# Kernel optimization log

Hardware: AMD Instinct MI355X
Metric: run time of the kernel (lower is better)

## Reference

```python
import jax, jax.numpy as jnp
import numpy as np

B, S, E, D, DE = 8, 128, 50, 300, 50  # batch, seq, edge_dim, gcn_dim, dep_embed_dim
EPS = 1e-6


def setup_inputs() -> dict:
    key = jax.random.key(0)
    ks = jax.random.split(key, 9)
    weight_prob_softmax = jax.nn.softmax(jax.random.normal(ks[0], (B, S, S, E)), axis=2)
    weight_adj = jax.random.normal(ks[1], (B, S, S, E))
    gcn_inputs = jax.random.normal(ks[2], (B, S, D))
    # self-loop added to adjacency after permute -> [B, E, S, S]; identity loops
    self_loop = jnp.broadcast_to(jnp.eye(S, dtype=jnp.float32), (B, E, S, S))
    W_w = jax.random.normal(ks[3], (D, D)) * 0.05          # gcn linear (in, out)
    W_b = jnp.zeros((D,))
    ln_a = jnp.ones((D,))
    ln_b = jnp.zeros((D,))
    refine_W = jax.random.normal(ks[4], (2 * D + 3 * E, DE)) * 0.05  # (750, 50)
    refine_b = jnp.zeros((DE,))
    return {
        "weight_prob_softmax": weight_prob_softmax,
        "weight_adj": weight_adj,
        "gcn_inputs": gcn_inputs,
        "self_loop": self_loop,
        "W_w": W_w, "W_b": W_b,
        "ln_a": ln_a, "ln_b": ln_b,
        "refine_W": refine_W, "refine_b": refine_b,
    }


def reference(weight_prob_softmax, weight_adj, gcn_inputs, self_loop,
              W_w, W_b, ln_a, ln_b, refine_W, refine_b):
    b, s, d = gcn_inputs.shape
    e = weight_prob_softmax.shape[-1]
    # [B,S,S,E] -> [B,E,S,S], add self loops
    wps = jnp.transpose(weight_prob_softmax, (0, 3, 1, 2)) + self_loop
    # per-relation-channel message passing: Ax[b,e,i,:] = sum_j wps[b,e,i,j] * x[b,j,:]
    Ax = jnp.einsum('beij,bjd->beid', wps, gcn_inputs)
    Ax = Ax.mean(axis=1)  # avg pooling over edge channels -> [B,S,D]
    h = Ax @ W_w + W_b
    # LayerNorm with unbiased std (torch x.std default) and (std + eps)
    mean = h.mean(axis=-1, keepdims=True)
    var_unbiased = jnp.sum((h - mean) ** 2, axis=-1, keepdims=True) / (d - 1)
    std = jnp.sqrt(var_unbiased)
    h = ln_a * (h - mean) / (std + EPS) + ln_b
    node = jax.nn.relu(h)  # [B,S,D]
    # node1[b,i,j] = node[b,j]; node2[b,i,j] = node[b,i]
    node1 = jnp.broadcast_to(node[:, None, :, :], (b, s, s, d))
    node2 = jnp.broadcast_to(node[:, :, None, :], (b, s, s, d))
    # diagonal edge features: [B,E,S] -> [B,S,E]
    diag = jnp.transpose(jnp.diagonal(weight_adj, axis1=1, axis2=2), (0, 2, 1))
    edge_i = jnp.broadcast_to(diag[:, None, :, :], (b, s, s, e))  # edge_i[b,i,j]=diag[b,j]
    edge_j = jnp.broadcast_to(diag[:, :, None, :], (b, s, s, e))  # edge_j[b,i,j]=diag[b,i]
    feat = jnp.concatenate([weight_adj, edge_i, edge_j, node1, node2], axis=-1)
    edge_out = feat @ refine_W + refine_b  # [B,S,S,DE]
    return node, edge_out
```

## Files before the change

kernel.cpp:

```cpp
#include <hip/hip_runtime.h>
#include <hip/hip_bf16.h>


typedef __bf16 bf16x8 __attribute__((ext_vector_type(8)));
typedef float f32x4 __attribute__((ext_vector_type(4)));
typedef float f32x2 __attribute__((ext_vector_type(2)));

__device__ __forceinline__ unsigned short f2bf(float f) {
    __hip_bfloat16 h = __float2bfloat16(f);
    union { __hip_bfloat16 h; unsigned short u; } c; c.h = h; return c.u;
}

__global__ void __launch_bounds__(1024, 8) k_node(
    const float* __restrict__ wps,
    const float* __restrict__ wa,
    const float* __restrict__ x,
    const float* __restrict__ Ww,
    const float* __restrict__ Wb,
    const float* __restrict__ lna,
    const float* __restrict__ lnb,
    const float* __restrict__ Rw,
    const float* __restrict__ rb,
    float* __restrict__ node_out,
    float* __restrict__ R1, float* __restrict__ R2)
{
    __shared__ __align__(16) float axp[6400];
    __shared__ __align__(16) float axm2[608];
    __shared__ __align__(16) float Mlt[256];
    __shared__ __align__(16) float srcL[704];
    __shared__ float red1[10], red2[10], stats[4];

    int tid = threadIdx.x;
    int row0 = blockIdx.x * 2;
    int b = row0 >> 7, i0 = row0 & 127;

    {
        const float2* p2 = (const float2*)(wps + (size_t)row0 * 6400);
        for (int idx = tid; idx < 6400; idx += 1024) {
            float2 v = p2[idx];
            axp[idx] = v.x + v.y;
        }
    }
    if (tid < 100) {
        int r = tid / 50, e = tid % 50;
        srcL[e * 2 + r] = wa[((size_t)(row0 + r) * 128 + (i0 + r)) * 50 + e];
    }
    __syncthreads();
    if (tid < 256) {
        int r = tid >> 7, j = tid & 127;
        const float* pp = &axp[tid * 25];
        float s = 0.f;
#pragma unroll
        for (int n = 0; n < 25; ++n) s += pp[n];
        Mlt[j * 2 + r] = s * (1.0f / 50.0f) + (((i0 + r) == j) ? 1.0f : 0.0f);
    }
    __syncthreads();

    int t = tid & 255, g = tid >> 8;
    bool has2 = (t < 44);
    int d1 = has2 ? 256 + t : 299;

    {
        f32x2 a0 = {0.f, 0.f}, a1 = {0.f, 0.f};
        const float* xp = x + (size_t)b * 38400;
        int j0 = g * 32;
#pragma unroll 8
        for (int jj = 0; jj < 32; ++jj) {
            int j = j0 + jj;
            f32x2 m2 = *(const f32x2*)&Mlt[j * 2];
            a0 += m2 * xp[j * 300 + t];
            a1 += m2 * xp[j * 300 + d1];
        }
        *(f32x2*)&axp[g * 608 + t * 2] = a0;
        if (has2) *(f32x2*)&axp[g * 608 + d1 * 2] = a1;
    }
    __syncthreads();
    if (tid < 300) {
        f32x2 s = *(f32x2*)&axp[tid * 2]        + *(f32x2*)&axp[608 + tid * 2]
                + *(f32x2*)&axp[1216 + tid * 2] + *(f32x2*)&axp[1824 + tid * 2];
        *(f32x2*)&axm2[tid * 2] = s;
    }
    __syncthreads();

    {
        f32x2 h0 = {0.f, 0.f}, h1 = {0.f, 0.f};
        int kb = g * 75, ke = kb + 75;
#pragma unroll 5
        for (int k = kb; k < ke; ++k) {
            f32x2 m2 = *(const f32x2*)&axm2[k * 2];
            h0 += m2 * Ww[k * 300 + t];
            h1 += m2 * Ww[k * 300 + d1];
        }
        *(f32x2*)&axp[g * 608 + t * 2] = h0;
        if (has2) *(f32x2*)&axp[g * 608 + d1 * 2] = h1;
    }
    __syncthreads();

    f32x2 hv = {0.f, 0.f};
    int wvi = tid >> 6, lane = tid & 63;
    if (tid < 320) {
        if (tid < 300) {
            hv = *(f32x2*)&axp[tid * 2]        + *(f32x2*)&axp[608 + tid * 2]
               + *(f32x2*)&axp[1216 + tid * 2] + *(f32x2*)&axp[1824 + tid * 2];
            hv += Wb[tid];
        }
        float s1r[2], s2r[2];
#pragma unroll
        for (int r = 0; r < 2; ++r) { s1r[r] = hv[r]; s2r[r] = hv[r] * hv[r]; }
        for (int off = 32; off; off >>= 1) {
#pragma unroll
            for (int r = 0; r < 2; ++r) {
                s1r[r] += __shfl_down(s1r[r], off);
                s2r[r] += __shfl_down(s2r[r], off);
            }
        }
        if (lane == 0) {
#pragma unroll
            for (int r = 0; r < 2; ++r) { red1[wvi * 2 + r] = s1r[r]; red2[wvi * 2 + r] = s2r[r]; }
        }
    }
    __syncthreads();
    if (tid < 2) {
        float s1 = 0.f, s2 = 0.f;
#pragma unroll
        for (int w = 0; w < 5; ++w) { s1 += red1[w * 2 + tid]; s2 += red2[w * 2 + tid]; }
        float mean = s1 * (1.0f / 300.0f);
        float var = (s2 - 300.0f * mean * mean) * (1.0f / 299.0f);
        var = fmaxf(var, 0.0f);
        stats[tid * 2] = mean;
        stats[tid * 2 + 1] = 1.0f / (sqrtf(var) + 1e-6f);
    }
    __syncthreads();

    if (tid < 300) {
        float la = lna[tid], lb = lnb[tid];
        f32x2 nv;
#pragma unroll
        for (int r = 0; r < 2; ++r) {
            float v = la * (hv[r] - stats[r * 2]) * stats[r * 2 + 1] + lb;
            v = fmaxf(v, 0.f);
            nv[r] = v;
            node_out[(size_t)(row0 + r) * 300 + tid] = v;
        }
        *(f32x2*)&srcL[(50 + tid) * 2] = nv;
    }
    __syncthreads();

    if (tid < 700) {
        int p = tid / 50, k = tid % 50;
        f32x2 r1a = {0.f, 0.f}, r2a = {0.f, 0.f};
        int ib = p * 25;
#pragma unroll 5
        for (int idx = ib; idx < ib + 25; ++idx) {
            f32x2 sv = *(const f32x2*)&srcL[idx * 2];
            float w1, w2;
            if (idx < 50) { w1 = Rw[(50 + idx) * 50 + k]; w2 = Rw[(100 + idx) * 50 + k]; }
            else { int d = idx - 50; w1 = Rw[(150 + d) * 50 + k]; w2 = Rw[(450 + d) * 50 + k]; }
            r1a += sv * w1;
            r2a += sv * w2;
        }
        *(f32x2*)&axp[(p * 50 + k) * 2] = r1a;
        *(f32x2*)&axp[2800 + (p * 50 + k) * 2] = r2a;
    }
    __syncthreads();
    if (tid < 100) {
        int r = tid / 50, k = tid % 50;
        float s1 = 0.f, s2 = rb[k];
#pragma unroll
        for (int p = 0; p < 14; ++p) {
            s1 += axp[(p * 50 + k) * 2 + r];
            s2 += axp[2800 + (p * 50 + k) * 2 + r];
        }
        R1[(size_t)(row0 + r) * 50 + k] = s1;
        R2[(size_t)(row0 + r) * 50 + k] = s2;
    }
}

__global__ void __launch_bounds__(256) k_edge(
    const float* __restrict__ wa,
    const float* __restrict__ Rw,
    const float* __restrict__ R1, const float* __restrict__ R2,
    float* __restrict__ eout)
{
    __shared__ __align__(16) unsigned char smem[27648];
    unsigned short* waA  = (unsigned short*)smem;
    unsigned short* rwBT = (unsigned short*)(smem + 18432);
    float* outF = (float*)smem;
    int tid = threadIdx.x;
    int bi = blockIdx.x;
    int b = bi >> 7;

    for (int idx = tid; idx < 2304; idx += 256) ((unsigned int*)rwBT)[idx] = 0u;
    for (int idx = tid; idx < 1408; idx += 256) {
        int j = idx / 11, c = idx % 11;
        *((unsigned int*)(waA + j * 72 + 50) + c) = 0u;
    }
    __syncthreads();

    const float2* wap = (const float2*)(wa + (size_t)bi * 6400);
    for (int idx = tid; idx < 3200; idx += 256) {
        float2 v = wap[idx];
        int f = idx * 2;
        int j = f / 50, e = f % 50;
        unsigned int pack = (unsigned int)f2bf(v.x) | ((unsigned int)f2bf(v.y) << 16);
        *(unsigned int*)(waA + j * 72 + e) = pack;
    }
    for (int idx = tid; idx < 2500; idx += 256) {
        int e = idx / 50, kk = idx % 50;
        rwBT[kk * 72 + e] = f2bf(Rw[idx]);
    }
    __syncthreads();

    int lane = tid & 63, wv = tid >> 6;
    int q = lane >> 4, lr = lane & 15;
    f32x4 acc[2][4] = {};

#pragma unroll
    for (int ks = 0; ks < 2; ++ks) {
        int e0 = ks * 32 + q * 8;
        bf16x8 a0 = *(const bf16x8*)&waA[(wv * 32 + lr) * 72 + e0];
        bf16x8 a1 = *(const bf16x8*)&waA[(wv * 32 + 16 + lr) * 72 + e0];
#pragma unroll
        for (int nt = 0; nt < 4; ++nt) {
            bf16x8 bb = *(const bf16x8*)&rwBT[(nt * 16 + lr) * 72 + e0];
            acc[0][nt] = __builtin_amdgcn_mfma_f32_16x16x32_bf16(a0, bb, acc[0][nt], 0, 0, 0);
            acc[1][nt] = __builtin_amdgcn_mfma_f32_16x16x32_bf16(a1, bb, acc[1][nt], 0, 0, 0);
        }
    }
    __syncthreads();

    const float* r2p = R2 + (size_t)bi * 50;
#pragma unroll
    for (int nt = 0; nt < 4; ++nt) {
        int kk = nt * 16 + lr;
        if (kk < 50) {
            float r2v = r2p[kk];
#pragma unroll
            for (int mi = 0; mi < 2; ++mi) {
                int jbase = wv * 32 + mi * 16 + q * 4;
#pragma unroll
                for (int r = 0; r < 4; ++r)
                    outF[(jbase + r) * 50 + kk] = acc[mi][nt][r] + r2v;
            }
        }
    }
    __syncthreads();

    const float4* R1b = (const float4*)(R1 + (size_t)b * 6400);
    const float4* L4  = (const float4*)outF;
    float4* op4 = (float4*)(eout + (size_t)bi * 6400);
    for (int f4 = tid; f4 < 1600; f4 += 256) {
        float4 v = L4[f4];
        float4 r = R1b[f4];
        v.x += r.x; v.y += r.y; v.z += r.z; v.w += r.w;
        op4[f4] = v;
    }
}

extern "C" void kernel_launch(void* const* d_in, const int* in_sizes, int n_in,
                              void* d_out, int out_size, void* d_ws, size_t ws_size,
                              hipStream_t stream)
{
    const float* wps = (const float*)d_in[0];
    const float* wa  = (const float*)d_in[1];
    const float* x   = (const float*)d_in[2];
    const float* Ww  = (const float*)d_in[4];
    const float* Wb  = (const float*)d_in[5];
    const float* lna = (const float*)d_in[6];
    const float* lnb = (const float*)d_in[7];
    const float* Rw  = (const float*)d_in[8];
    const float* rb  = (const float*)d_in[9];

    float* R1 = (float*)d_ws;
    float* R2 = ((float*)d_ws) + 51200;

    float* node_out = (float*)d_out;
    float* edge_out = node_out + 307200;

    k_node<<<512, 1024, 0, stream>>>(wps, wa, x, Ww, Wb, lna, lnb, Rw, rb,
                                     node_out, R1, R2);
    k_edge<<<1024, 256, 0, stream>>>(wa, Rw, R1, R2, edge_out);
}
```

Measured before the change: 153.7 us.

## Precompute bf16 refine weights once and load A fragments directly from global

One block of k_node now converts and transposes the refine weight slice into a padded bf16 layout in workspace. k_edge copies that ready-made layout into shared memory and no longer zero-fills or converts the weights per block. It also builds the MFMA A fragments straight from global fp32 weight_adj rows, dropping the shared-memory staging pass and one barrier. In exchange, global reads are unaligned and per-lane strided (rows of 50 floats), and the last k_node block does a little extra work.

```diff
diff --git a/kernel.cpp b/kernel.cpp
--- a/kernel.cpp
+++ b/kernel.cpp
@@ -5,10 +5,29 @@
 typedef __bf16 bf16x8 __attribute__((ext_vector_type(8)));
 typedef float f32x4 __attribute__((ext_vector_type(4)));
 typedef float f32x2 __attribute__((ext_vector_type(2)));
+typedef float f32x4_u __attribute__((ext_vector_type(4))) __attribute__((aligned(4)));
 
 __device__ __forceinline__ unsigned short f2bf(float f) {
     __hip_bfloat16 h = __float2bfloat16(f);
     union { __hip_bfloat16 h; unsigned short u; } c; c.h = h; return c.u;
+}
+
+__device__ __forceinline__ bf16x8 fragA(const float* __restrict__ ap, int e0) {
+    union { bf16x8 v; unsigned short u[8]; } c;
+    if (e0 <= 40) {
+        f32x4_u v0 = *(const f32x4_u*)(ap + e0);
+        f32x4_u v1 = *(const f32x4_u*)(ap + e0 + 4);
+#pragma unroll
+        for (int i = 0; i < 4; ++i) { c.u[i] = f2bf(v0[i]); c.u[4 + i] = f2bf(v1[i]); }
+    } else if (e0 == 48) {
+        c.u[0] = f2bf(ap[48]); c.u[1] = f2bf(ap[49]);
+#pragma unroll
+        for (int i = 2; i < 8; ++i) c.u[i] = 0;
+    } else {
+#pragma unroll
+        for (int i = 0; i < 8; ++i) c.u[i] = 0;
+    }
+    return c.v;
 }
 
 __global__ void __launch_bounds__(1024, 8) k_node(
@@ -22,7 +41,8 @@
     const float* __restrict__ Rw,
     const float* __restrict__ rb,
     float* __restrict__ node_out,
-    float* __restrict__ R1, float* __restrict__ R2)
+    float* __restrict__ R1, float* __restrict__ R2,
+    unsigned short* __restrict__ rwPre)
 {
     __shared__ __align__(16) float axp[6400];
     __shared__ __align__(16) float axm2[608];
@@ -33,6 +53,13 @@
     int tid = threadIdx.x;
     int row0 = blockIdx.x * 2;
     int b = row0 >> 7, i0 = row0 & 127;
+
+    if (blockIdx.x == 511) {
+        for (int idx = tid; idx < 4608; idx += 1024) {
+            int kk = idx / 72, e = idx % 72;
+            rwPre[idx] = (kk < 50 && e < 50) ? f2bf(Rw[e * 50 + kk]) : (unsigned short)0;
+        }
+    }
 
     {
         const float2* p2 = (const float2*)(wps + (size_t)row0 * 6400);
@@ -178,53 +205,38 @@
 
 __global__ void __launch_bounds__(256) k_edge(
     const float* __restrict__ wa,
-    const float* __restrict__ Rw,
+    const unsigned int* __restrict__ rwPre,
     const float* __restrict__ R1, const float* __restrict__ R2,
     float* __restrict__ eout)
 {
-    __shared__ __align__(16) unsigned char smem[27648];
-    unsigned short* waA  = (unsigned short*)smem;
-    unsigned short* rwBT = (unsigned short*)(smem + 18432);
+    __shared__ __align__(16) unsigned char smem[25600];
+    unsigned short* rwBT = (unsigned short*)smem;
     float* outF = (float*)smem;
     int tid = threadIdx.x;
     int bi = blockIdx.x;
     int b = bi >> 7;
 
-    for (int idx = tid; idx < 2304; idx += 256) ((unsigned int*)rwBT)[idx] = 0u;
-    for (int idx = tid; idx < 1408; idx += 256) {
-        int j = idx / 11, c = idx % 11;
-        *((unsigned int*)(waA + j * 72 + 50) + c) = 0u;
-    }
-    __syncthreads();
-
-    const float2* wap = (const float2*)(wa + (size_t)bi * 6400);
-    for (int idx = tid; idx < 3200; idx += 256) {
-        float2 v = wap[idx];
-        int f = idx * 2;
-        int j = f / 50, e = f % 50;
-        unsigned int pack = (unsigned int)f2bf(v.x) | ((unsigned int)f2bf(v.y) << 16);
-        *(unsigned int*)(waA + j * 72 + e) = pack;
-    }
-    for (int idx = tid; idx < 2500; idx += 256) {
-        int e = idx / 50, kk = idx % 50;
-        rwBT[kk * 72 + e] = f2bf(Rw[idx]);
-    }
+    for (int idx = tid; idx < 2304; idx += 256)
+        ((unsigned int*)rwBT)[idx] = rwPre[idx];
     __syncthreads();
 
     int lane = tid & 63, wv = tid >> 6;
     int q = lane >> 4, lr = lane & 15;
+    const float* wab = wa + (size_t)bi * 6400;
     f32x4 acc[2][4] = {};
 
 #pragma unroll
-    for (int ks = 0; ks < 2; ++ks) {
-        int e0 = ks * 32 + q * 8;
-        bf16x8 a0 = *(const bf16x8*)&waA[(wv * 32 + lr) * 72 + e0];
-        bf16x8 a1 = *(const bf16x8*)&waA[(wv * 32 + 16 + lr) * 72 + e0];
-#pragma unroll
-        for (int nt = 0; nt < 4; ++nt) {
-            bf16x8 bb = *(const bf16x8*)&rwBT[(nt * 16 + lr) * 72 + e0];
-            acc[0][nt] = __builtin_amdgcn_mfma_f32_16x16x32_bf16(a0, bb, acc[0][nt], 0, 0, 0);
-            acc[1][nt] = __builtin_amdgcn_mfma_f32_16x16x32_bf16(a1, bb, acc[1][nt], 0, 0, 0);
+    for (int mi = 0; mi < 2; ++mi) {
+        const float* ap = wab + (wv * 32 + mi * 16 + lr) * 50;
+#pragma unroll
+        for (int ks = 0; ks < 2; ++ks) {
+            int e0 = ks * 32 + q * 8;
+            bf16x8 a = fragA(ap, e0);
+#pragma unroll
+            for (int nt = 0; nt < 4; ++nt) {
+                bf16x8 bb = *(const bf16x8*)&rwBT[(nt * 16 + lr) * 72 + e0];
+                acc[mi][nt] = __builtin_amdgcn_mfma_f32_16x16x32_bf16(a, bb, acc[mi][nt], 0, 0, 0);
+            }
         }
     }
     __syncthreads();
@@ -273,11 +285,13 @@
 
     float* R1 = (float*)d_ws;
     float* R2 = ((float*)d_ws) + 51200;
+    unsigned short* rwPre16 = (unsigned short*)(((float*)d_ws) + 102400);
+    const unsigned int* rwPre32 = (const unsigned int*)rwPre16;
 
     float* node_out = (float*)d_out;
     float* edge_out = node_out + 307200;
 
     k_node<<<512, 1024, 0, stream>>>(wps, wa, x, Ww, Wb, lna, lnb, Rw, rb,
-                                     node_out, R1, R2);
-    k_edge<<<1024, 256, 0, stream>>>(wa, Rw, R1, R2, edge_out);
-}
+                                     node_out, R1, R2, rwPre16);
+    k_edge<<<1024, 256, 0, stream>>>(wa, rwPre32, R1, R2, edge_out);
+}
```

Measured after the change: 153.8 us. Within noise of the previous version (+0.1%).
